# Kernel tuning notes

Measured on AMD Instinct MI355X. Metric: run time of the kernel, lower is better.

Reference implementation:

```python
import jax, jax.numpy as jnp
import numpy as np

IMG_SIZE = 1280
STRIDE = 4
NUM_CLASSES = 80
TOPK = 1000
NMS_THRESH = 0.6
SCALE_CLAMP = float(np.log(1000.0))  # DEFAULT_SCALE_CLAMP
N_ANCHORS = (IMG_SIZE // STRIDE) ** 2  # 102400


def _anchors():
    # generate_anchors: meshgrid over fmp, stacked as (x, y), flattened
    fmp = IMG_SIZE // STRIDE
    ys, xs = jnp.meshgrid(jnp.arange(fmp), jnp.arange(fmp), indexing='ij')
    return jnp.stack([xs, ys], axis=-1).reshape(-1, 2).astype(jnp.float32)


def _decode_boxes(anchors, reg):
    # [wl, ht, wr, hb] -> [x1, y1, x2, y2], scaled by stride
    reg = jnp.exp(jnp.minimum(reg, SCALE_CLAMP))
    xy1 = anchors - reg[..., :2]
    xy2 = anchors + reg[..., 2:]
    return jnp.concatenate([xy1, xy2], axis=-1) * STRIDE


def _iou_matrix(b):
    # pairwise IoU with the exact eps handling of the original numpy NMS
    x1, y1, x2, y2 = b[:, 0], b[:, 1], b[:, 2], b[:, 3]
    areas = (x2 - x1) * (y2 - y1)
    xx1 = jnp.maximum(x1[:, None], x1[None, :])
    yy1 = jnp.maximum(y1[:, None], y1[None, :])
    xx2 = jnp.minimum(x2[:, None], x2[None, :])
    yy2 = jnp.minimum(y2[:, None], y2[None, :])
    w = jnp.maximum(1e-10, xx2 - xx1)
    h = jnp.maximum(1e-10, yy2 - yy1)
    inter = w * h
    return inter / (areas[:, None] + areas[None, :] - inter + 1e-10)


def _greedy_nms(iou, same_class):
    # boxes are pre-sorted by score descending (top_k output order), so a
    # single greedy pass with a same-class mask is equivalent to the
    # original per-class loop (each class subset preserves score order).
    K = iou.shape[0]
    suppress = (iou > NMS_THRESH) & same_class
    idx = jnp.arange(K)

    def body(keep, i):
        row = suppress[i] & keep[i]  # only a kept box suppresses others
        keep = keep & ~(row & (idx > i))
        return keep, None

    keep0 = jnp.ones((K,), dtype=bool)
    keep, _ = jax.lax.scan(body, keep0, idx)
    return keep


def setup_inputs() -> dict:
    key = jax.random.key(0)
    k1, k2, k3 = jax.random.split(key, 3)
    hmp_pred = jax.random.normal(k1, (N_ANCHORS, NUM_CLASSES), dtype=jnp.float32)
    reg_pred = jax.random.normal(k2, (N_ANCHORS, 4), dtype=jnp.float32)
    iou_pred = jax.random.normal(k3, (N_ANCHORS, 1), dtype=jnp.float32)
    return {"hmp_pred": hmp_pred, "reg_pred": reg_pred, "iou_pred": iou_pred}


def reference(hmp_pred, reg_pred, iou_pred):
    # score fusion: sqrt(sigmoid(hmp) * sigmoid(iou)), max over classes
    fused = jnp.sqrt(jax.nn.sigmoid(hmp_pred) * jax.nn.sigmoid(iou_pred))  # [N, C]
    scores = jnp.max(fused, axis=-1)
    labels = jnp.argmax(fused, axis=-1)

    # top-k selection (sorted descending)
    scores, indices = jax.lax.top_k(scores, TOPK)
    labels = labels[indices]
    reg = reg_pred[indices]
    anc = _anchors()[indices]

    # decode + normalize + clamp
    bboxes = jnp.clip(_decode_boxes(anc, reg) / IMG_SIZE, 0.0, 1.0)  # [K, 4]

    # class-aware greedy NMS; keep mask replaces the dynamic-shape filter
    same_class = labels[:, None] == labels[None, :]
    keep = _greedy_nms(_iou_matrix(bboxes), same_class)
    return scores, labels, bboxes, keep
```

## Files before the change

kernel.cpp:

```cpp
#include <hip/hip_runtime.h>
#include <stdint.h>

#define N_ANCH 102400
#define FMP 320
#define K_TOP 1000
#define NMS_T 0.6f
#define SC_CLAMP 6.907755278982137f
#define IMGF 1280.0f
#define NBINS 16384

#define OFF_SCORES   0u
#define OFF_LABELS   409600u
#define OFF_HIST     819200u
#define OFF_META     884736u
#define OFF_KEYS     884992u
#define OFF_BOXES    917760u
#define OFF_LAB1K    933760u
#define OFF_MASK     937760u
#define OFF_DIAG     1065760u

__device__ __forceinline__ float sigf(float x) {
    return 1.0f / (1.0f + expf(-x));
}

__global__ __launch_bounds__(256) void k_scores(const float* __restrict__ hmp,
                                                const float* __restrict__ iou,
                                                float* __restrict__ scores,
                                                uint32_t* __restrict__ labels,
                                                uint32_t* __restrict__ hist,
                                                uint32_t* __restrict__ meta,
                                                uint64_t* __restrict__ diag) {
    int blk = blockIdx.x;
    if (blk < 64) {
        hist[blk * 256 + threadIdx.x] = 0u;
    } else if (blk == 64) {
        if (threadIdx.x < 64) meta[threadIdx.x] = 0u;
#pragma unroll
        for (int k = 0; k < 4; ++k) diag[threadIdx.x * 4 + k] = 0ull;
    }
    int gid = blk * 256 + threadIdx.x;
    int a = gid >> 2;
    int q = gid & 3;
    float si = sigf(iou[a]);
    const float4* row4 = (const float4*)hmp + (size_t)a * 20 + q;
    float4 v[5];
#pragma unroll
    for (int j = 0; j < 5; ++j) v[j] = row4[j * 4];
    float best = -1.0f;
    int bc = 0;
#pragma unroll
    for (int j = 0; j < 5; ++j) {
        int cb = j * 16 + q * 4;
        float f;
        f = sqrtf(sigf(v[j].x) * si); if (f > best) { best = f; bc = cb; }
        f = sqrtf(sigf(v[j].y) * si); if (f > best) { best = f; bc = cb + 1; }
        f = sqrtf(sigf(v[j].z) * si); if (f > best) { best = f; bc = cb + 2; }
        f = sqrtf(sigf(v[j].w) * si); if (f > best) { best = f; bc = cb + 3; }
    }
#pragma unroll
    for (int off = 1; off <= 2; off <<= 1) {
        float of = __shfl_xor(best, off);
        int   oc = __shfl_xor(bc, off);
        if (of > best || (of == best && oc < bc)) { best = of; bc = oc; }
    }
    if (q == 0) {
        scores[a] = best;
        labels[a] = (uint32_t)bc;
    }
}

__global__ __launch_bounds__(1024) void k_hist(const float* __restrict__ scores,
                                               uint32_t* __restrict__ hist,
                                               uint32_t* __restrict__ meta) {
    __shared__ uint32_t lh[NBINS];
    __shared__ int lastFlag;
    for (int i = threadIdx.x; i < NBINS; i += 1024) lh[i] = 0u;
    __syncthreads();
    int base = blockIdx.x * 1600;
    for (int k = threadIdx.x; k < 1600; k += 1024) {
        uint32_t bin = __float_as_uint(scores[base + k]) >> 16;
        atomicAdd(&lh[bin], 1u);
    }
    __syncthreads();
    for (int i = threadIdx.x; i < NBINS; i += 1024) {
        uint32_t c = lh[i];
        if (c) atomicAdd(&hist[i], c);
    }
    __threadfence();
    __syncthreads();
    if (threadIdx.x == 0) lastFlag = (atomicAdd(&meta[8], 1u) == 63u);
    __syncthreads();
    if (!lastFlag) return;
    __threadfence();
    int t = threadIdx.x;
    uint32_t s = 0;
#pragma unroll
    for (int b = 0; b < 16; ++b) s += hist[t * 16 + b];
    lh[t] = s;
    __syncthreads();
    for (int off = 1; off < 1024; off <<= 1) {
        uint32_t v = lh[t] + ((t + off < 1024) ? lh[t + off] : 0u);
        __syncthreads();
        lh[t] = v;
        __syncthreads();
    }
    uint32_t inc   = lh[t];
    uint32_t above = (t < 1023) ? lh[t + 1] : 0u;
    if (above < K_TOP && inc >= K_TOP) {
        uint32_t loc[16];
#pragma unroll
        for (int b = 0; b < 16; ++b) loc[b] = hist[t * 16 + b];
        uint32_t cnt = above;
        for (int b = 15; b >= 0; --b) {
            cnt += loc[b];
            if (cnt >= K_TOP) { meta[0] = (uint32_t)(t * 16 + b); break; }
        }
    }
}

__global__ __launch_bounds__(256) void k_collect(const float* __restrict__ scores,
                                                 uint32_t* __restrict__ meta,
                                                 uint64_t* __restrict__ keys) {
    __shared__ uint32_t cnt, base;
    if (threadIdx.x == 0) cnt = 0u;
    __syncthreads();
    int i = blockIdx.x * 256 + threadIdx.x;
    uint32_t bits = __float_as_uint(scores[i]);
    bool cand = (bits >> 16) >= meta[0];
    uint32_t pos = 0;
    if (cand) pos = atomicAdd(&cnt, 1u);
    __syncthreads();
    if (threadIdx.x == 0 && cnt) base = atomicAdd(&meta[2], cnt);
    __syncthreads();
    if (cand) {
        uint32_t p = base + pos;
        if (p < 4096u)
            keys[p] = ((uint64_t)bits << 32) | (uint64_t)(0xFFFFFFFFu - (uint32_t)i);
    }
}

__global__ __launch_bounds__(1024) void k_rank(const uint64_t* __restrict__ keys,
                                               const uint32_t* __restrict__ meta,
                                               const uint32_t* __restrict__ labels,
                                               const float* __restrict__ reg,
                                               float* __restrict__ out,
                                               float* __restrict__ boxes,
                                               uint32_t* __restrict__ lab1k) {
    __shared__ uint64_t sk[4096];
    uint32_t M = meta[2];
    if (M > 4096u) M = 4096u;
    if ((uint32_t)(blockIdx.x * 16) >= M) return;
    for (uint32_t i = threadIdx.x; i < M; i += 1024) sk[i] = keys[i];
    __syncthreads();
    int lane = threadIdx.x & 63;
    int wg = blockIdx.x * 16 + (threadIdx.x >> 6);
    if ((uint32_t)wg >= M) return;
    uint64_t mykey = sk[wg];
    uint32_t rank = 0;
    for (uint32_t j = lane; j < M; j += 64) rank += (sk[j] > mykey) ? 1u : 0u;
#pragma unroll
    for (int off = 32; off; off >>= 1) rank += __shfl_xor(rank, off);
    if (lane != 0 || rank >= K_TOP) return;
    int t = (int)rank;
    uint32_t sbits = (uint32_t)(mykey >> 32);
    uint32_t idx   = 0xFFFFFFFFu - (uint32_t)(mykey & 0xFFFFFFFFull);
    float score = __uint_as_float(sbits);
    uint32_t lab = labels[idx];
    out[t]         = score;
    out[K_TOP + t] = (float)lab;
    lab1k[t]       = lab;
    float ax = (float)(idx % FMP);
    float ay = (float)(idx / FMP);
    float4 rr = ((const float4*)reg)[idx];
    float e0 = expf(fminf(rr.x, SC_CLAMP));
    float e1 = expf(fminf(rr.y, SC_CLAMP));
    float e2 = expf(fminf(rr.z, SC_CLAMP));
    float e3 = expf(fminf(rr.w, SC_CLAMP));
    float x1 = fminf(fmaxf((ax - e0) * 4.0f / IMGF, 0.0f), 1.0f);
    float y1 = fminf(fmaxf((ay - e1) * 4.0f / IMGF, 0.0f), 1.0f);
    float x2 = fminf(fmaxf((ax + e2) * 4.0f / IMGF, 0.0f), 1.0f);
    float y2 = fminf(fmaxf((ay + e3) * 4.0f / IMGF, 0.0f), 1.0f);
    out[2 * K_TOP + t * 4 + 0] = x1;
    out[2 * K_TOP + t * 4 + 1] = y1;
    out[2 * K_TOP + t * 4 + 2] = x2;
    out[2 * K_TOP + t * 4 + 3] = y2;
    boxes[t * 4 + 0] = x1;
    boxes[t * 4 + 1] = y1;
    boxes[t * 4 + 2] = x2;
    boxes[t * 4 + 3] = y2;
}

__global__ __launch_bounds__(1024) void k_mask(const float* __restrict__ boxes,
                                               const uint32_t* __restrict__ lab1k,
                                               uint64_t* __restrict__ mask,
                                               uint64_t* __restrict__ diag) {
    int r = blockIdx.x * 16 + (threadIdx.x >> 6);
    int lane = threadIdx.x & 63;
    if (r >= K_TOP) return;
    float4 bi = ((const float4*)boxes)[r];
    uint32_t li = lab1k[r];
    float areai = (bi.z - bi.x) * (bi.w - bi.y);
    int iw = r >> 6;
    uint64_t dw = 0ull;
#pragma unroll
    for (int w = 0; w < 16; ++w) {
        int j = w * 64 + lane;
        bool sup = false;
        if (j < K_TOP && j > r) {
            float4 bj = ((const float4*)boxes)[j];
            float areaj = (bj.z - bj.x) * (bj.w - bj.y);
            float xx1 = fmaxf(bi.x, bj.x);
            float yy1 = fmaxf(bi.y, bj.y);
            float xx2 = fminf(bi.z, bj.z);
            float yy2 = fminf(bi.w, bj.w);
            float ww = fmaxf(1e-10f, xx2 - xx1);
            float hh = fmaxf(1e-10f, yy2 - yy1);
            float inter = ww * hh;
            float iouv = inter / (areai + areaj - inter + 1e-10f);
            sup = (iouv > NMS_T) && (li == lab1k[j]);
        }
        unsigned long long m = __ballot(sup);
        if (lane == 0) mask[(size_t)r * 16 + w] = (uint64_t)m;
        if (w == iw) dw = (uint64_t)m;
    }
    if (lane == 0) diag[r] = dw;
}

__global__ __launch_bounds__(64, 1) void k_scan(const uint64_t* __restrict__ mask,
                                                const uint64_t* __restrict__ diag,
                                                float* __restrict__ out) {
    int lane = threadIdx.x;
    int q = lane >> 4, wrd = lane & 15;
    uint64_t remv = 0ull;
    uint64_t dcur = diag[lane];
    for (int g = 0; g < 16; ++g) {
        uint64_t dnxt = (g < 15) ? diag[64 * (g + 1) + lane] : 0ull;
        uint64_t bun[16];
        if (g < 15) {
#pragma unroll
            for (int r4 = 0; r4 < 16; ++r4)
                bun[r4] = mask[(size_t)(64 * g + 4 * r4 + q) * 16 + wrd];
        }
        uint32_t dlo = 0, dhi = 0;
#pragma unroll
        for (int qq = 0; qq < 4; ++qq) {
            dlo |= __builtin_amdgcn_readlane((uint32_t)remv, qq * 16 + g);
            dhi |= __builtin_amdgcn_readlane((uint32_t)(remv >> 32), qq * 16 + g);
        }
        uint64_t D = ((uint64_t)dhi << 32) | dlo;
#pragma unroll
        for (int b = 0; b < 64; ++b) {
            uint32_t tlo = __builtin_amdgcn_readlane((uint32_t)dcur, b);
            uint32_t thi = __builtin_amdgcn_readlane((uint32_t)(dcur >> 32), b);
            uint64_t T = ((uint64_t)thi << 32) | tlo;
            uint64_t sel = ((D >> b) & 1ull) - 1ull;
            D |= T & sel;
        }
        uint64_t keepg = ~D;
        int j = g * 64 + lane;
        if (j < K_TOP) out[6 * K_TOP + j] = (float)((keepg >> lane) & 1ull);
        if (g < 15) {
#pragma unroll
            for (int r4 = 0; r4 < 16; ++r4) {
                uint32_t kb = (uint32_t)(keepg >> (4 * r4 + q)) & 1u;
                uint64_t mm = 0ull - (uint64_t)kb;
                remv |= bun[r4] & mm;
            }
        }
        dcur = dnxt;
    }
}

extern "C" void kernel_launch(void* const* d_in, const int* in_sizes, int n_in,
                              void* d_out, int out_size, void* d_ws, size_t ws_size,
                              hipStream_t stream) {
    const float* hmp = (const float*)d_in[0];
    const float* reg = (const float*)d_in[1];
    const float* iou = (const float*)d_in[2];
    float* out = (float*)d_out;
    char* ws = (char*)d_ws;

    float*    scores = (float*)(ws + OFF_SCORES);
    uint32_t* labels = (uint32_t*)(ws + OFF_LABELS);
    uint32_t* hist   = (uint32_t*)(ws + OFF_HIST);
    uint32_t* meta   = (uint32_t*)(ws + OFF_META);
    uint64_t* keys   = (uint64_t*)(ws + OFF_KEYS);
    float*    boxes  = (float*)(ws + OFF_BOXES);
    uint32_t* lab1k  = (uint32_t*)(ws + OFF_LAB1K);
    uint64_t* mask   = (uint64_t*)(ws + OFF_MASK);
    uint64_t* diag   = (uint64_t*)(ws + OFF_DIAG);

    k_scores<<<dim3(N_ANCH * 4 / 256), dim3(256), 0, stream>>>(hmp, iou, scores, labels, hist, meta, diag);
    k_hist<<<dim3(64), dim3(1024), 0, stream>>>(scores, hist, meta);
    k_collect<<<dim3(N_ANCH / 256), dim3(256), 0, stream>>>(scores, meta, keys);
    k_rank<<<dim3(256), dim3(1024), 0, stream>>>(keys, meta, labels, reg, out, boxes, lab1k);
    k_mask<<<dim3(63), dim3(1024), 0, stream>>>(boxes, lab1k, mask, diag);
    k_scan<<<dim3(1), dim3(64), 0, stream>>>(mask, diag, out);
}
```

Before: 155.8 us.

## Fuse histogram, collect, rank and mask kernels into one persistent kernel with grid barriers

Merges the four middle kernels (histogram/threshold, candidate collect, rank/decode, IoU mask) into a single 64-block persistent kernel. Blocks spin on the cutoff published by the last histogram block and use software grid barriers between phases. This removes three kernel launch gaps and their drain/fill overhead. In exchange it relies on all 64 blocks being co-resident, spins on atomics, and the rank phase now runs on 64 blocks instead of 256.

```diff
diff --git a/kernel.cpp b/kernel.cpp
--- a/kernel.cpp
+++ b/kernel.cpp
@@ -21,6 +21,24 @@
 
 __device__ __forceinline__ float sigf(float x) {
     return 1.0f / (1.0f + expf(-x));
+}
+
+__device__ __forceinline__ void grid_bar(uint32_t* cnt, uint32_t* gen, uint32_t nblk) {
+    __syncthreads();
+    if (threadIdx.x == 0) {
+        __threadfence();
+        uint32_t g = __hip_atomic_load(gen, __ATOMIC_ACQUIRE, __HIP_MEMORY_SCOPE_AGENT);
+        uint32_t a = __hip_atomic_fetch_add(cnt, 1u, __ATOMIC_ACQ_REL, __HIP_MEMORY_SCOPE_AGENT);
+        if (a == nblk - 1u) {
+            __hip_atomic_store(cnt, 0u, __ATOMIC_RELAXED, __HIP_MEMORY_SCOPE_AGENT);
+            __hip_atomic_fetch_add(gen, 1u, __ATOMIC_ACQ_REL, __HIP_MEMORY_SCOPE_AGENT);
+        } else {
+            while (__hip_atomic_load(gen, __ATOMIC_ACQUIRE, __HIP_MEMORY_SCOPE_AGENT) == g)
+                __builtin_amdgcn_s_sleep(2);
+        }
+        __threadfence();
+    }
+    __syncthreads();
 }
 
 __global__ __launch_bounds__(256) void k_scores(const float* __restrict__ hmp,
@@ -34,7 +52,7 @@
     if (blk < 64) {
         hist[blk * 256 + threadIdx.x] = 0u;
     } else if (blk == 64) {
-        if (threadIdx.x < 64) meta[threadIdx.x] = 0u;
+        if (threadIdx.x < 64) meta[threadIdx.x] = (threadIdx.x == 0) ? 0xFFFFFFFFu : 0u;
 #pragma unroll
         for (int k = 0; k < 4; ++k) diag[threadIdx.x * 4 + k] = 0ull;
     }
@@ -69,161 +87,185 @@
     }
 }
 
-__global__ __launch_bounds__(1024) void k_hist(const float* __restrict__ scores,
-                                               uint32_t* __restrict__ hist,
-                                               uint32_t* __restrict__ meta) {
-    __shared__ uint32_t lh[NBINS];
+__global__ __launch_bounds__(1024, 4) void k_mid(const float* __restrict__ scores,
+                                                 const uint32_t* __restrict__ labels,
+                                                 const float* __restrict__ reg,
+                                                 uint32_t* __restrict__ hist,
+                                                 uint32_t* __restrict__ meta,
+                                                 uint64_t* __restrict__ keys,
+                                                 float* __restrict__ out,
+                                                 float* __restrict__ boxes,
+                                                 uint32_t* __restrict__ lab1k,
+                                                 uint64_t* __restrict__ mask,
+                                                 uint64_t* __restrict__ diag) {
+    __shared__ union SMU { uint32_t h[NBINS]; uint64_t kk[4096]; } sm;
+    __shared__ uint32_t s_cut, ccnt, cbase;
     __shared__ int lastFlag;
-    for (int i = threadIdx.x; i < NBINS; i += 1024) lh[i] = 0u;
-    __syncthreads();
-    int base = blockIdx.x * 1600;
-    for (int k = threadIdx.x; k < 1600; k += 1024) {
-        uint32_t bin = __float_as_uint(scores[base + k]) >> 16;
-        atomicAdd(&lh[bin], 1u);
-    }
-    __syncthreads();
-    for (int i = threadIdx.x; i < NBINS; i += 1024) {
-        uint32_t c = lh[i];
+
+    const int tid = threadIdx.x;
+    const int blk = blockIdx.x;
+    const int lane = tid & 63;
+
+    for (int i = tid; i < NBINS; i += 1024) sm.h[i] = 0u;
+    __syncthreads();
+    {
+        int base = blk * 1600;
+        for (int k = tid; k < 1600; k += 1024) {
+            uint32_t bin = __float_as_uint(scores[base + k]) >> 16;
+            atomicAdd(&sm.h[bin], 1u);
+        }
+    }
+    __syncthreads();
+    for (int i = tid; i < NBINS; i += 1024) {
+        uint32_t c = sm.h[i];
         if (c) atomicAdd(&hist[i], c);
     }
     __threadfence();
     __syncthreads();
-    if (threadIdx.x == 0) lastFlag = (atomicAdd(&meta[8], 1u) == 63u);
-    __syncthreads();
-    if (!lastFlag) return;
-    __threadfence();
-    int t = threadIdx.x;
-    uint32_t s = 0;
-#pragma unroll
-    for (int b = 0; b < 16; ++b) s += hist[t * 16 + b];
-    lh[t] = s;
-    __syncthreads();
-    for (int off = 1; off < 1024; off <<= 1) {
-        uint32_t v = lh[t] + ((t + off < 1024) ? lh[t + off] : 0u);
+    if (tid == 0) lastFlag = (atomicAdd(&meta[8], 1u) == 63u);
+    __syncthreads();
+    if (lastFlag) {
+        __threadfence();
+        int t = tid;
+        uint32_t s = 0;
+#pragma unroll
+        for (int b = 0; b < 16; ++b) s += hist[t * 16 + b];
+        sm.h[t] = s;
         __syncthreads();
-        lh[t] = v;
-        __syncthreads();
-    }
-    uint32_t inc   = lh[t];
-    uint32_t above = (t < 1023) ? lh[t + 1] : 0u;
-    if (above < K_TOP && inc >= K_TOP) {
-        uint32_t loc[16];
-#pragma unroll
-        for (int b = 0; b < 16; ++b) loc[b] = hist[t * 16 + b];
-        uint32_t cnt = above;
-        for (int b = 15; b >= 0; --b) {
-            cnt += loc[b];
-            if (cnt >= K_TOP) { meta[0] = (uint32_t)(t * 16 + b); break; }
-        }
-    }
-}
-
-__global__ __launch_bounds__(256) void k_collect(const float* __restrict__ scores,
-                                                 uint32_t* __restrict__ meta,
-                                                 uint64_t* __restrict__ keys) {
-    __shared__ uint32_t cnt, base;
-    if (threadIdx.x == 0) cnt = 0u;
-    __syncthreads();
-    int i = blockIdx.x * 256 + threadIdx.x;
-    uint32_t bits = __float_as_uint(scores[i]);
-    bool cand = (bits >> 16) >= meta[0];
-    uint32_t pos = 0;
-    if (cand) pos = atomicAdd(&cnt, 1u);
-    __syncthreads();
-    if (threadIdx.x == 0 && cnt) base = atomicAdd(&meta[2], cnt);
-    __syncthreads();
-    if (cand) {
-        uint32_t p = base + pos;
+        for (int off = 1; off < 1024; off <<= 1) {
+            uint32_t v = sm.h[t] + ((t + off < 1024) ? sm.h[t + off] : 0u);
+            __syncthreads();
+            sm.h[t] = v;
+            __syncthreads();
+        }
+        uint32_t inc   = sm.h[t];
+        uint32_t above = (t < 1023) ? sm.h[t + 1] : 0u;
+        if (above < K_TOP && inc >= K_TOP) {
+            uint32_t loc[16];
+#pragma unroll
+            for (int b = 0; b < 16; ++b) loc[b] = hist[t * 16 + b];
+            uint32_t cnt = above;
+            for (int b = 15; b >= 0; --b) {
+                cnt += loc[b];
+                if (cnt >= K_TOP) {
+                    __hip_atomic_store(&meta[0], (uint32_t)(t * 16 + b),
+                                       __ATOMIC_RELEASE, __HIP_MEMORY_SCOPE_AGENT);
+                    break;
+                }
+            }
+        }
+    }
+    if (tid == 0) {
+        uint32_t c;
+        while ((c = __hip_atomic_load(&meta[0], __ATOMIC_ACQUIRE, __HIP_MEMORY_SCOPE_AGENT)) == 0xFFFFFFFFu)
+            __builtin_amdgcn_s_sleep(2);
+        s_cut = c;
+        ccnt = 0u;
+    }
+    __syncthreads();
+
+    uint32_t mybits[2], myi[2], mypos[2];
+    int nc = 0;
+    {
+        uint32_t cut = s_cut;
+        int base = blk * 1600;
+        for (int k = tid; k < 1600; k += 1024) {
+            int i = base + k;
+            uint32_t bits = __float_as_uint(scores[i]);
+            if ((bits >> 16) >= cut) {
+                mypos[nc] = atomicAdd(&ccnt, 1u);
+                mybits[nc] = bits;
+                myi[nc] = (uint32_t)i;
+                ++nc;
+            }
+        }
+    }
+    __syncthreads();
+    if (tid == 0) cbase = ccnt ? atomicAdd(&meta[2], ccnt) : 0u;
+    __syncthreads();
+    for (int c = 0; c < nc; ++c) {
+        uint32_t p = cbase + mypos[c];
         if (p < 4096u)
-            keys[p] = ((uint64_t)bits << 32) | (uint64_t)(0xFFFFFFFFu - (uint32_t)i);
-    }
-}
-
-__global__ __launch_bounds__(1024) void k_rank(const uint64_t* __restrict__ keys,
-                                               const uint32_t* __restrict__ meta,
-                                               const uint32_t* __restrict__ labels,
-                                               const float* __restrict__ reg,
-                                               float* __restrict__ out,
-                                               float* __restrict__ boxes,
-                                               uint32_t* __restrict__ lab1k) {
-    __shared__ uint64_t sk[4096];
+            keys[p] = ((uint64_t)mybits[c] << 32) | (uint64_t)(0xFFFFFFFFu - myi[c]);
+    }
+
+    grid_bar(&meta[16], &meta[17], 64u);
+
     uint32_t M = meta[2];
     if (M > 4096u) M = 4096u;
-    if ((uint32_t)(blockIdx.x * 16) >= M) return;
-    for (uint32_t i = threadIdx.x; i < M; i += 1024) sk[i] = keys[i];
-    __syncthreads();
-    int lane = threadIdx.x & 63;
-    int wg = blockIdx.x * 16 + (threadIdx.x >> 6);
-    if ((uint32_t)wg >= M) return;
-    uint64_t mykey = sk[wg];
-    uint32_t rank = 0;
-    for (uint32_t j = lane; j < M; j += 64) rank += (sk[j] > mykey) ? 1u : 0u;
-#pragma unroll
-    for (int off = 32; off; off >>= 1) rank += __shfl_xor(rank, off);
-    if (lane != 0 || rank >= K_TOP) return;
-    int t = (int)rank;
-    uint32_t sbits = (uint32_t)(mykey >> 32);
-    uint32_t idx   = 0xFFFFFFFFu - (uint32_t)(mykey & 0xFFFFFFFFull);
-    float score = __uint_as_float(sbits);
-    uint32_t lab = labels[idx];
-    out[t]         = score;
-    out[K_TOP + t] = (float)lab;
-    lab1k[t]       = lab;
-    float ax = (float)(idx % FMP);
-    float ay = (float)(idx / FMP);
-    float4 rr = ((const float4*)reg)[idx];
-    float e0 = expf(fminf(rr.x, SC_CLAMP));
-    float e1 = expf(fminf(rr.y, SC_CLAMP));
-    float e2 = expf(fminf(rr.z, SC_CLAMP));
-    float e3 = expf(fminf(rr.w, SC_CLAMP));
-    float x1 = fminf(fmaxf((ax - e0) * 4.0f / IMGF, 0.0f), 1.0f);
-    float y1 = fminf(fmaxf((ay - e1) * 4.0f / IMGF, 0.0f), 1.0f);
-    float x2 = fminf(fmaxf((ax + e2) * 4.0f / IMGF, 0.0f), 1.0f);
-    float y2 = fminf(fmaxf((ay + e3) * 4.0f / IMGF, 0.0f), 1.0f);
-    out[2 * K_TOP + t * 4 + 0] = x1;
-    out[2 * K_TOP + t * 4 + 1] = y1;
-    out[2 * K_TOP + t * 4 + 2] = x2;
-    out[2 * K_TOP + t * 4 + 3] = y2;
-    boxes[t * 4 + 0] = x1;
-    boxes[t * 4 + 1] = y1;
-    boxes[t * 4 + 2] = x2;
-    boxes[t * 4 + 3] = y2;
-}
-
-__global__ __launch_bounds__(1024) void k_mask(const float* __restrict__ boxes,
-                                               const uint32_t* __restrict__ lab1k,
-                                               uint64_t* __restrict__ mask,
-                                               uint64_t* __restrict__ diag) {
-    int r = blockIdx.x * 16 + (threadIdx.x >> 6);
-    int lane = threadIdx.x & 63;
-    if (r >= K_TOP) return;
-    float4 bi = ((const float4*)boxes)[r];
-    uint32_t li = lab1k[r];
-    float areai = (bi.z - bi.x) * (bi.w - bi.y);
-    int iw = r >> 6;
-    uint64_t dw = 0ull;
-#pragma unroll
-    for (int w = 0; w < 16; ++w) {
-        int j = w * 64 + lane;
-        bool sup = false;
-        if (j < K_TOP && j > r) {
-            float4 bj = ((const float4*)boxes)[j];
-            float areaj = (bj.z - bj.x) * (bj.w - bj.y);
-            float xx1 = fmaxf(bi.x, bj.x);
-            float yy1 = fmaxf(bi.y, bj.y);
-            float xx2 = fminf(bi.z, bj.z);
-            float yy2 = fminf(bi.w, bj.w);
-            float ww = fmaxf(1e-10f, xx2 - xx1);
-            float hh = fmaxf(1e-10f, yy2 - yy1);
-            float inter = ww * hh;
-            float iouv = inter / (areai + areaj - inter + 1e-10f);
-            sup = (iouv > NMS_T) && (li == lab1k[j]);
-        }
-        unsigned long long m = __ballot(sup);
-        if (lane == 0) mask[(size_t)r * 16 + w] = (uint64_t)m;
-        if (w == iw) dw = (uint64_t)m;
-    }
-    if (lane == 0) diag[r] = dw;
+    if ((uint32_t)(blk * 16) < M) {
+        for (uint32_t i = tid; i < M; i += 1024) sm.kk[i] = keys[i];
+        __syncthreads();
+        for (uint32_t wg = (uint32_t)(blk * 16 + (tid >> 6)); wg < M; wg += 1024u) {
+            uint64_t mykey = sm.kk[wg];
+            uint32_t rank = 0;
+            for (uint32_t j = lane; j < M; j += 64) rank += (sm.kk[j] > mykey) ? 1u : 0u;
+#pragma unroll
+            for (int off = 32; off; off >>= 1) rank += __shfl_xor(rank, off);
+            if (lane == 0 && rank < K_TOP) {
+                int t = (int)rank;
+                uint32_t sbits = (uint32_t)(mykey >> 32);
+                uint32_t idx   = 0xFFFFFFFFu - (uint32_t)(mykey & 0xFFFFFFFFull);
+                float score = __uint_as_float(sbits);
+                uint32_t lab = labels[idx];
+                out[t]         = score;
+                out[K_TOP + t] = (float)lab;
+                lab1k[t]       = lab;
+                float ax = (float)(idx % FMP);
+                float ay = (float)(idx / FMP);
+                float4 rr = ((const float4*)reg)[idx];
+                float e0 = expf(fminf(rr.x, SC_CLAMP));
+                float e1 = expf(fminf(rr.y, SC_CLAMP));
+                float e2 = expf(fminf(rr.z, SC_CLAMP));
+                float e3 = expf(fminf(rr.w, SC_CLAMP));
+                float x1 = fminf(fmaxf((ax - e0) * 4.0f / IMGF, 0.0f), 1.0f);
+                float y1 = fminf(fmaxf((ay - e1) * 4.0f / IMGF, 0.0f), 1.0f);
+                float x2 = fminf(fmaxf((ax + e2) * 4.0f / IMGF, 0.0f), 1.0f);
+                float y2 = fminf(fmaxf((ay + e3) * 4.0f / IMGF, 0.0f), 1.0f);
+                out[2 * K_TOP + t * 4 + 0] = x1;
+                out[2 * K_TOP + t * 4 + 1] = y1;
+                out[2 * K_TOP + t * 4 + 2] = x2;
+                out[2 * K_TOP + t * 4 + 3] = y2;
+                boxes[t * 4 + 0] = x1;
+                boxes[t * 4 + 1] = y1;
+                boxes[t * 4 + 2] = x2;
+                boxes[t * 4 + 3] = y2;
+            }
+        }
+    }
+
+    grid_bar(&meta[16], &meta[17], 64u);
+
+    int r = blk * 16 + (tid >> 6);
+    if (r < K_TOP) {
+        float4 bi = ((const float4*)boxes)[r];
+        uint32_t li = lab1k[r];
+        float areai = (bi.z - bi.x) * (bi.w - bi.y);
+        int iw = r >> 6;
+        uint64_t dw = 0ull;
+#pragma unroll
+        for (int w = 0; w < 16; ++w) {
+            int j = w * 64 + lane;
+            bool sup = false;
+            if (j < K_TOP && j > r) {
+                float4 bj = ((const float4*)boxes)[j];
+                float areaj = (bj.z - bj.x) * (bj.w - bj.y);
+                float xx1 = fmaxf(bi.x, bj.x);
+                float yy1 = fmaxf(bi.y, bj.y);
+                float xx2 = fminf(bi.z, bj.z);
+                float yy2 = fminf(bi.w, bj.w);
+                float ww = fmaxf(1e-10f, xx2 - xx1);
+                float hh = fmaxf(1e-10f, yy2 - yy1);
+                float inter = ww * hh;
+                float iouv = inter / (areai + areaj - inter + 1e-10f);
+                sup = (iouv > NMS_T) && (li == lab1k[j]);
+            }
+            unsigned long long m = __ballot(sup);
+            if (lane == 0) mask[(size_t)r * 16 + w] = (uint64_t)m;
+            if (w == iw) dw = (uint64_t)m;
+        }
+        if (lane == 0) diag[r] = dw;
+    }
 }
 
 __global__ __launch_bounds__(64, 1) void k_scan(const uint64_t* __restrict__ mask,
@@ -291,9 +333,6 @@
     uint64_t* diag   = (uint64_t*)(ws + OFF_DIAG);
 
     k_scores<<<dim3(N_ANCH * 4 / 256), dim3(256), 0, stream>>>(hmp, iou, scores, labels, hist, meta, diag);
-    k_hist<<<dim3(64), dim3(1024), 0, stream>>>(scores, hist, meta);
-    k_collect<<<dim3(N_ANCH / 256), dim3(256), 0, stream>>>(scores, meta, keys);
-    k_rank<<<dim3(256), dim3(1024), 0, stream>>>(keys, meta, labels, reg, out, boxes, lab1k);
-    k_mask<<<dim3(63), dim3(1024), 0, stream>>>(boxes, lab1k, mask, diag);
+    k_mid<<<dim3(64), dim3(1024), 0, stream>>>(scores, labels, reg, hist, meta, keys, out, boxes, lab1k, mask, diag);
     k_scan<<<dim3(1), dim3(64), 0, stream>>>(mask, diag, out);
 }
```

Result: slower. 175.8 us (+12.8%).

## Fuse histogram threshold and candidate collection into one single-block kernel

Applied to the files above, without the earlier changes.

Replaces the 64-block global histogram kernel and the 400-block collect kernel with one 1024-thread single-block kernel. It builds the full 16384-bin histogram in LDS, finds the cutoff bin, then rescans all scores to gather candidates through an LDS counter. This drops a kernel launch, the global histogram zeroing and merging, and the global atomics. The trade-off is that both passes over 100K scores now run on a single CU, with heavy LDS atomic contention on the few hot bins, which may serialize the work.

```diff
diff --git a/kernel.cpp b/kernel.cpp
--- a/kernel.cpp
+++ b/kernel.cpp
@@ -11,7 +11,6 @@
 
 #define OFF_SCORES   0u
 #define OFF_LABELS   409600u
-#define OFF_HIST     819200u
 #define OFF_META     884736u
 #define OFF_KEYS     884992u
 #define OFF_BOXES    917760u
@@ -27,14 +26,9 @@
                                                 const float* __restrict__ iou,
                                                 float* __restrict__ scores,
                                                 uint32_t* __restrict__ labels,
-                                                uint32_t* __restrict__ hist,
-                                                uint32_t* __restrict__ meta,
                                                 uint64_t* __restrict__ diag) {
     int blk = blockIdx.x;
-    if (blk < 64) {
-        hist[blk * 256 + threadIdx.x] = 0u;
-    } else if (blk == 64) {
-        if (threadIdx.x < 64) meta[threadIdx.x] = 0u;
+    if (blk == 0) {
 #pragma unroll
         for (int k = 0; k < 4; ++k) diag[threadIdx.x * 4 + k] = 0ull;
     }
@@ -69,74 +63,71 @@
     }
 }
 
-__global__ __launch_bounds__(1024) void k_hist(const float* __restrict__ scores,
-                                               uint32_t* __restrict__ hist,
-                                               uint32_t* __restrict__ meta) {
+__global__ __launch_bounds__(1024) void k_histcollect(const float* __restrict__ scores,
+                                                      uint32_t* __restrict__ meta,
+                                                      uint64_t* __restrict__ keys) {
     __shared__ uint32_t lh[NBINS];
-    __shared__ int lastFlag;
-    for (int i = threadIdx.x; i < NBINS; i += 1024) lh[i] = 0u;
-    __syncthreads();
-    int base = blockIdx.x * 1600;
-    for (int k = threadIdx.x; k < 1600; k += 1024) {
-        uint32_t bin = __float_as_uint(scores[base + k]) >> 16;
-        atomicAdd(&lh[bin], 1u);
-    }
-    __syncthreads();
-    for (int i = threadIdx.x; i < NBINS; i += 1024) {
-        uint32_t c = lh[i];
-        if (c) atomicAdd(&hist[i], c);
-    }
-    __threadfence();
-    __syncthreads();
-    if (threadIdx.x == 0) lastFlag = (atomicAdd(&meta[8], 1u) == 63u);
-    __syncthreads();
-    if (!lastFlag) return;
-    __threadfence();
-    int t = threadIdx.x;
-    uint32_t s = 0;
-#pragma unroll
-    for (int b = 0; b < 16; ++b) s += hist[t * 16 + b];
-    lh[t] = s;
+    __shared__ uint32_t coarse[1024];
+    __shared__ uint32_t s_cut, ccnt;
+
+    const int tid = threadIdx.x;
+    for (int i = tid; i < NBINS; i += 1024) lh[i] = 0u;
+    if (tid == 0) { ccnt = 0u; s_cut = 0u; }
+    __syncthreads();
+
+    const float4* s4 = (const float4*)scores;
+    for (int k = tid; k < N_ANCH / 4; k += 1024) {
+        float4 v = s4[k];
+        atomicAdd(&lh[__float_as_uint(v.x) >> 16], 1u);
+        atomicAdd(&lh[__float_as_uint(v.y) >> 16], 1u);
+        atomicAdd(&lh[__float_as_uint(v.z) >> 16], 1u);
+        atomicAdd(&lh[__float_as_uint(v.w) >> 16], 1u);
+    }
+    __syncthreads();
+
+    {
+        uint32_t s = 0;
+#pragma unroll
+        for (int b = 0; b < 16; ++b) s += lh[tid * 16 + b];
+        coarse[tid] = s;
+    }
     __syncthreads();
     for (int off = 1; off < 1024; off <<= 1) {
-        uint32_t v = lh[t] + ((t + off < 1024) ? lh[t + off] : 0u);
+        uint32_t v = coarse[tid] + ((tid + off < 1024) ? coarse[tid + off] : 0u);
         __syncthreads();
-        lh[t] = v;
+        coarse[tid] = v;
         __syncthreads();
     }
-    uint32_t inc   = lh[t];
-    uint32_t above = (t < 1023) ? lh[t + 1] : 0u;
-    if (above < K_TOP && inc >= K_TOP) {
-        uint32_t loc[16];
-#pragma unroll
-        for (int b = 0; b < 16; ++b) loc[b] = hist[t * 16 + b];
-        uint32_t cnt = above;
-        for (int b = 15; b >= 0; --b) {
-            cnt += loc[b];
-            if (cnt >= K_TOP) { meta[0] = (uint32_t)(t * 16 + b); break; }
-        }
-    }
-}
-
-__global__ __launch_bounds__(256) void k_collect(const float* __restrict__ scores,
-                                                 uint32_t* __restrict__ meta,
-                                                 uint64_t* __restrict__ keys) {
-    __shared__ uint32_t cnt, base;
-    if (threadIdx.x == 0) cnt = 0u;
-    __syncthreads();
-    int i = blockIdx.x * 256 + threadIdx.x;
-    uint32_t bits = __float_as_uint(scores[i]);
-    bool cand = (bits >> 16) >= meta[0];
-    uint32_t pos = 0;
-    if (cand) pos = atomicAdd(&cnt, 1u);
-    __syncthreads();
-    if (threadIdx.x == 0 && cnt) base = atomicAdd(&meta[2], cnt);
-    __syncthreads();
-    if (cand) {
-        uint32_t p = base + pos;
-        if (p < 4096u)
-            keys[p] = ((uint64_t)bits << 32) | (uint64_t)(0xFFFFFFFFu - (uint32_t)i);
-    }
+    {
+        uint32_t inc   = coarse[tid];
+        uint32_t above = (tid < 1023) ? coarse[tid + 1] : 0u;
+        if (above < K_TOP && inc >= K_TOP) {
+            uint32_t cnt = above;
+            for (int b = 15; b >= 0; --b) {
+                cnt += lh[tid * 16 + b];
+                if (cnt >= K_TOP) { s_cut = (uint32_t)(tid * 16 + b); break; }
+            }
+        }
+    }
+    __syncthreads();
+
+    const uint32_t cut = s_cut;
+    for (int k = tid; k < N_ANCH / 4; k += 1024) {
+        float4 v = s4[k];
+        uint32_t bb[4] = { __float_as_uint(v.x), __float_as_uint(v.y),
+                           __float_as_uint(v.z), __float_as_uint(v.w) };
+#pragma unroll
+        for (int c = 0; c < 4; ++c) {
+            if ((bb[c] >> 16) >= cut) {
+                uint32_t p = atomicAdd(&ccnt, 1u);
+                if (p < 4096u)
+                    keys[p] = ((uint64_t)bb[c] << 32) |
+                              (uint64_t)(0xFFFFFFFFu - (uint32_t)(k * 4 + c));
+            }
+        }
+    }
+    __syncthreads();
+    if (tid == 0) meta[2] = ccnt;
 }
 
 __global__ __launch_bounds__(1024) void k_rank(const uint64_t* __restrict__ keys,
@@ -282,7 +273,6 @@
 
     float*    scores = (float*)(ws + OFF_SCORES);
     uint32_t* labels = (uint32_t*)(ws + OFF_LABELS);
-    uint32_t* hist   = (uint32_t*)(ws + OFF_HIST);
     uint32_t* meta   = (uint32_t*)(ws + OFF_META);
     uint64_t* keys   = (uint64_t*)(ws + OFF_KEYS);
     float*    boxes  = (float*)(ws + OFF_BOXES);
@@ -290,9 +280,8 @@
     uint64_t* mask   = (uint64_t*)(ws + OFF_MASK);
     uint64_t* diag   = (uint64_t*)(ws + OFF_DIAG);
 
-    k_scores<<<dim3(N_ANCH * 4 / 256), dim3(256), 0, stream>>>(hmp, iou, scores, labels, hist, meta, diag);
-    k_hist<<<dim3(64), dim3(1024), 0, stream>>>(scores, hist, meta);
-    k_collect<<<dim3(N_ANCH / 256), dim3(256), 0, stream>>>(scores, meta, keys);
+    k_scores<<<dim3(N_ANCH * 4 / 256), dim3(256), 0, stream>>>(hmp, iou, scores, labels, diag);
+    k_histcollect<<<dim3(1), dim3(1024), 0, stream>>>(scores, meta, keys);
     k_rank<<<dim3(256), dim3(1024), 0, stream>>>(keys, meta, labels, reg, out, boxes, lab1k);
     k_mask<<<dim3(63), dim3(1024), 0, stream>>>(boxes, lab1k, mask, diag);
     k_scan<<<dim3(1), dim3(64), 0, stream>>>(mask, diag, out);
```

Result: faster. 148.6 us (-4.6%).
